# Performance work log

Hardware: AMD Instinct MI355X
Metric: run time of the kernel (lower is better)

## Reference

```python
import jax, jax.numpy as jnp
import numpy as np

BS, IN, HID, LAT, OUT = 8192, 48, 256, 64, 128
CAT = LAT + OUT + HID  # LSTM input size = 448


def setup_inputs() -> dict:
    key = jax.random.key(0)
    ks = jax.random.split(key, 13)
    s = 0.02
    return {
        "x": jax.random.normal(ks[0], (BS, IN), jnp.float32),
        "enc": jax.random.normal(ks[1], (BS, HID), jnp.float32),
        "z": jax.random.normal(ks[2], (BS, LAT), jnp.float32),
        "W_ih": jax.random.normal(ks[3], (4 * OUT, CAT), jnp.float32) * s,
        "W_hh": jax.random.normal(ks[4], (4 * OUT, OUT), jnp.float32) * s,
        "b_ih": jax.random.normal(ks[5], (4 * OUT,), jnp.float32) * s,
        "b_hh": jax.random.normal(ks[6], (4 * OUT,), jnp.float32) * s,
        "W_u0": jax.random.normal(ks[7], (OUT, IN), jnp.float32) * s,
        "b_u0": jax.random.normal(ks[8], (OUT,), jnp.float32) * s,
        "W_h1": jax.random.normal(ks[9], (OUT, CAT), jnp.float32) * s,
        "b_h1": jax.random.normal(ks[10], (OUT,), jnp.float32) * s,
        "W_h2": jax.random.normal(ks[11], (OUT, CAT), jnp.float32) * s,
        "b_h2": jax.random.normal(ks[12], (OUT,), jnp.float32) * s,
        "horizon": 50,
    }


def reference(x, enc, z, W_ih, W_hh, b_ih, b_hh, W_u0, b_u0, W_h1, b_h1, W_h2, b_h2, horizon):
    # initial input u0 = Linear(input_size -> output_size)(x)
    u0 = x @ W_u0.T + b_u0                       # [bs, OUT]
    xi0 = jnp.concatenate([z, u0, enc], axis=-1)  # [bs, CAT]
    h0 = xi0 @ W_h1.T + b_h1                     # LSTM hidden init [bs, OUT]
    c0 = xi0 @ W_h2.T + b_h2                     # LSTM cell init   [bs, OUT]
    b = b_ih + b_hh

    def step(carry, _):
        h, c, yi = carry
        xi = jnp.concatenate([z, yi, enc], axis=-1)   # [bs, CAT]
        gates = xi @ W_ih.T + h @ W_hh.T + b          # [bs, 4*OUT]
        i_g, f_g, g_g, o_g = jnp.split(gates, 4, axis=-1)  # torch order: i,f,g,o
        c_new = jax.nn.sigmoid(f_g) * c + jax.nn.sigmoid(i_g) * jnp.tanh(g_g)
        h_new = jax.nn.sigmoid(o_g) * jnp.tanh(c_new)
        return (h_new, c_new, h_new), h_new

    _, ys = jax.lax.scan(step, (h0, c0, u0), None, length=horizon)  # [T, bs, OUT]
    # torch stacks yi [bs, 1, OUT] along dim=1 -> [bs, T, 1, OUT]
    return jnp.transpose(ys, (1, 0, 2))[:, :, None, :]
```

## Files before the change

### kernel.cpp

```cpp
#include <hip/hip_runtime.h>
#include <stdint.h>

typedef short bf16x8 __attribute__((ext_vector_type(8)));
typedef float f32x4 __attribute__((ext_vector_type(4)));
typedef unsigned short u16x4 __attribute__((ext_vector_type(4)));

#define MFMA16(a,b,c) __builtin_amdgcn_mfma_f32_16x16x32_bf16((a),(b),(c),0,0,0)

__device__ __forceinline__ unsigned short bf16_rne(float f){
  unsigned int u = __builtin_bit_cast(unsigned int, f);
  return (unsigned short)((u + 0x7FFFu + ((u>>16)&1u)) >> 16);
}
__device__ __forceinline__ float bf16_f(unsigned short h){
  unsigned int u = ((unsigned int)h) << 16;
  return __builtin_bit_cast(float, u);
}

#define SZ_WINIT (48*24*512*2)
#define OFF_W0   (SZ_WINIT)
#define SZ_W0    (32*12*512*2)
#define OFF_WC   (OFF_W0 + SZ_W0)
#define SZ_WC    (32*8*512*2)
#define OFF_BIAS (OFF_WC + SZ_WC)
#define OFF_XQ   (OFF_BIAS + 4096)
#define OFF_XH   (OFF_XQ + 512*49*4)

__global__ __launch_bounds__(256)
void decoder_compose(const float* __restrict__ W_ih, const float* __restrict__ W_u0,
                     const float* __restrict__ b_u0, const float* __restrict__ W_h1,
                     const float* __restrict__ W_h2, float* __restrict__ ws){
  __shared__ float wu[128][49];
  __shared__ float wrow[16][128];
  float* Xq = (float*)((char*)ws + OFF_XQ);
  float* Xh = (float*)((char*)ws + OFF_XH);
  const int b = blockIdx.x, tid = threadIdx.x;
  for (int i = tid; i < 128*49; i += 256){
    int c = i/49, j = i - c*49;
    wu[c][j] = (j < 48) ? W_u0[c*48 + j] : b_u0[c];
  }
  for (int i = tid; i < 16*128; i += 256){
    int r = i>>7, c = i&127;
    const float* src;
    if (b < 32) src = W_ih + (b*16 + r)*448 + 64;
    else { int mm = (b-32)*16 + r; src = (mm<128) ? (W_h1 + mm*448 + 64) : (W_h2 + (mm-128)*448 + 64); }
    wrow[r][c] = src[c];
  }
  __syncthreads();
  for (int o = tid; o < 16*49; o += 256){
    int r = o/49, j = o - r*49;
    float s = 0.f;
    #pragma unroll 8
    for (int c = 0; c < 128; ++c) s += wrow[r][c]*wu[c][j];
    if (b < 32) Xq[(b*16+r)*49 + j] = s;
    else        Xh[((b-32)*16+r)*49 + j] = s;
  }
}

__global__ __launch_bounds__(256)
void decoder_pack(const float* __restrict__ W_ih, const float* __restrict__ W_hh,
                  const float* __restrict__ b_ih, const float* __restrict__ b_hh,
                  const float* __restrict__ W_h1, const float* __restrict__ W_h2,
                  const float* __restrict__ b_h1, const float* __restrict__ b_h2,
                  unsigned short* __restrict__ wsu, float* __restrict__ ws){
  const float* Xq = (const float*)((const char*)ws + OFF_XQ);
  const float* Xh = (const float*)((const char*)ws + OFF_XH);
  float* bias = (float*)((char*)ws + OFF_BIAS);
  const int gid = blockIdx.x*256 + threadIdx.x;
  const int slot = gid >> 6, lane = gid & 63;
  const int n16 = lane & 15, p = lane >> 4;

  float v[8];
  unsigned short* dh; unsigned short* dl;
  if (slot < 576) {
    int nt = slot/12, kt = slot - nt*12;
    int n = nt*16 + n16;
    #pragma unroll
    for (int j=0;j<8;++j){
      int k = kt*32 + p*8 + j;
      float xv = 0.f;
      if (n < 256) {
        const float* W = (n<128) ? (W_h1 + n*448) : (W_h2 + (n-128)*448);
        if (k < 64) xv = W[k];
        else if (k < 320) xv = W[192 + k - 64];
        else if (k < 368) xv = Xh[n*49 + (k-320)];
      } else {
        int m = n - 256;
        if (k < 64) xv = W_ih[m*448 + k];
        else if (k < 320) xv = W_ih[m*448 + 192 + k - 64];
      }
      v[j] = xv;
    }
    dh = wsu + ((nt*24 + kt)*64 + lane)*8;
    dl = wsu + ((nt*24 + 12 + kt)*64 + lane)*8;
  } else if (slot < 768) {
    int s2 = slot - 576;
    int nt = s2/6, kt = s2 - nt*6;
    int n = nt*16 + n16;
    #pragma unroll
    for (int j=0;j<8;++j){
      int k = kt*32 + p*8 + j;
      float xv = 0.f;
      if (k < 49)      xv = Xq[n*49 + k];
      else if (k >= 64) xv = W_hh[n*128 + k - 64];
      v[j] = xv;
    }
    unsigned short* b = wsu + OFF_W0/2;
    dh = b + ((nt*12 + kt)*64 + lane)*8;
    dl = b + ((nt*12 + 6 + kt)*64 + lane)*8;
  } else if (slot < 896) {
    int s3 = slot - 768;
    int nt = s3>>2, kt = s3&3;
    int n = nt*16 + n16;
    #pragma unroll
    for (int j=0;j<8;++j){
      int k = kt*32 + p*8 + j;
      v[j] = W_ih[n*448 + 64 + k] + W_hh[n*128 + k];
    }
    unsigned short* b = wsu + OFF_WC/2;
    dh = b + ((nt*8 + kt)*64 + lane)*8;
    dl = b + ((nt*8 + 4 + kt)*64 + lane)*8;
  } else {
    int i = gid - 896*64;
    if (i < 768) {
      float bv;
      if (i < 128)      bv = b_h1[i] + Xh[i*49 + 48];
      else if (i < 256) bv = b_h2[i-128] + Xh[i*49 + 48];
      else              bv = b_ih[i-256] + b_hh[i-256];
      bias[i] = bv;
    }
    return;
  }
  bf16x8 vh, vl;
  #pragma unroll
  for (int j=0;j<8;++j){
    unsigned short h = bf16_rne(v[j]);
    vh[j] = (short)h;
    vl[j] = (short)bf16_rne(v[j] - bf16_f(h));
  }
  *(bf16x8*)dh = vh;
  *(bf16x8*)dl = vl;
}

#define LDS_A0H 0
#define LDS_A0L 12288
#define LDS_XIH 24576
#define LDS_XIL 49152
#define LDS_H   24576
#define LDS_TOTAL 73728

__global__ __launch_bounds__(512, 2)
void decoder_main(const float* __restrict__ x, const float* __restrict__ enc, const float* __restrict__ z,
                  const unsigned short* __restrict__ wsu, const float* __restrict__ bias,
                  const int* __restrict__ hz, float* __restrict__ out){
  extern __shared__ char smem[];
  const int tid = threadIdx.x;
  const int w = tid>>6, lane = tid&63, n16 = lane&15, p = lane>>4;
  const int p16 = p*16;
  const int R0 = blockIdx.x*32;
  const int T = hz[0];

  for (int i = tid; i < 32*384; i += 512){
    int r = i/384, c = i - r*384;
    float v;
    if (c < 64)       v = z[(R0+r)*64 + c];
    else if (c < 320) v = enc[(R0+r)*256 + c - 64];
    else if (c < 368) v = x[(R0+r)*48 + c - 320];
    else              v = 0.f;
    unsigned short h = bf16_rne(v);
    int off = r*768 + ((2*c) ^ ((r&7)<<4));
    *(unsigned short*)(smem + LDS_XIH + off) = h;
    *(unsigned short*)(smem + LDS_XIL + off) = bf16_rne(v - bf16_f(h));
  }
  for (int i = tid; i < 32*64; i += 512){
    int r = i>>6, c = i&63;
    float v = (c < 48) ? x[(R0+r)*48 + c] : (c == 48 ? 1.f : 0.f);
    unsigned short h = bf16_rne(v);
    int off = r*384 + ((2*c) ^ ((r&7)<<4));
    *(unsigned short*)(smem + LDS_A0H + off) = h;
    *(unsigned short*)(smem + LDS_A0L + off) = bf16_rne(v - bf16_f(h));
  }
  __syncthreads();

  const int row0 = n16, row1 = 16 + n16;
  const int s0 = (row0&7)<<4, s1 = (row1&7)<<4;

  f32x4 accs[6][2];
  #pragma unroll
  for (int i=0;i<6;++i){
    int nt = (i==0) ? w : (i==1) ? (8+w) : (16 + 8*(i-2) + w);
    f32x4 bv = *(const f32x4*)(bias + nt*16 + p*4);
    accs[i][0] = bv; accs[i][1] = bv;
  }
  #pragma unroll
  for (int kt=0; kt<12; ++kt){
    bf16x8 bh0 = *(const bf16x8*)(smem + LDS_XIH + row0*768 + ((kt*64 + p16) ^ s0));
    bf16x8 bh1 = *(const bf16x8*)(smem + LDS_XIH + row1*768 + ((kt*64 + p16) ^ s1));
    bf16x8 bl0 = *(const bf16x8*)(smem + LDS_XIL + row0*768 + ((kt*64 + p16) ^ s0));
    bf16x8 bl1 = *(const bf16x8*)(smem + LDS_XIL + row1*768 + ((kt*64 + p16) ^ s1));
    bf16x8 wa[6], wl[6];
    #pragma unroll
    for (int i=0;i<6;++i){
      if (kt >= 10 && i >= 2) continue;
      int nt = (i==0) ? w : (i==1) ? (8+w) : (16 + 8*(i-2) + w);
      wa[i] = *(const bf16x8*)(wsu + ((nt*24 + kt)*64 + lane)*8);
      wl[i] = *(const bf16x8*)(wsu + ((nt*24 + 12 + kt)*64 + lane)*8);
    }
    #pragma unroll
    for (int i=0;i<6;++i){ if (kt >= 10 && i >= 2) continue;
      accs[i][0] = MFMA16(wa[i], bh0, accs[i][0]);
      accs[i][1] = MFMA16(wa[i], bh1, accs[i][1]); }
    #pragma unroll
    for (int i=0;i<6;++i){ if (kt >= 10 && i >= 2) continue;
      accs[i][0] = MFMA16(wa[i], bl0, accs[i][0]);
      accs[i][1] = MFMA16(wa[i], bl1, accs[i][1]); }
    #pragma unroll
    for (int i=0;i<6;++i){ if (kt >= 10 && i >= 2) continue;
      accs[i][0] = MFMA16(wl[i], bh0, accs[i][0]);
      accs[i][1] = MFMA16(wl[i], bh1, accs[i][1]); }
  }
  __syncthreads();

  #pragma unroll
  for (int bt=0; bt<2; ++bt){
    int row = bt*16 + n16, s = (row&7)<<4;
    u16x4 vh, vl;
    #pragma unroll
    for (int e=0;e<4;++e){
      float hv = accs[0][bt][e];
      unsigned short h = bf16_rne(hv);
      vh[e] = h; vl[e] = bf16_rne(hv - bf16_f(h));
    }
    int off = row*384 + ((128 + 32*w + 8*p) ^ s);
    *(u16x4*)(smem + LDS_A0H + off) = vh;
    *(u16x4*)(smem + LDS_A0L + off) = vl;
  }
  f32x4 creg[2] = { accs[1][0], accs[1][1] };
  f32x4 base_r[2][4];
  #pragma unroll
  for (int q=0;q<4;++q){ base_r[0][q] = accs[2+q][0]; base_r[1][q] = accs[2+q][1]; }
  __syncthreads();

  float* outp0 = out + (size_t)(R0 + n16)      * (size_t)(T*128) + (16*w + 4*p);
  float* outp1 = out + (size_t)(R0 + 16 + n16) * (size_t)(T*128) + (16*w + 4*p);

  f32x4 acc[2][4];
  f32x4 hcur0, hcur1;
  const float K1 = 1.44269504088896340736f;
  const float K2 = 2.88539008177792681472f;

  auto lstm_tail = [&](int wb){
    #pragma unroll
    for (int bt=0; bt<2; ++bt){
      f32x4 hh;
      #pragma unroll
      for (int e=0;e<4;++e){
        float iv = acc[bt][0][e], fv = acc[bt][1][e], gv = acc[bt][2][e], ov = acc[bt][3][e];
        float c = creg[bt][e];
        float ef = __builtin_amdgcn_exp2f(-K1*fv);
        float sf = __builtin_amdgcn_rcpf(1.f + ef);
        float ei = __builtin_amdgcn_exp2f(-K1*iv);
        float eg = __builtin_amdgcn_exp2f(-K2*gv);
        float d  = __builtin_amdgcn_rcpf((1.f+ei)*(1.f+eg));
        c = sf*c + (1.f-eg)*d;
        float eo = __builtin_amdgcn_exp2f(-K1*ov);
        float ec = __builtin_amdgcn_exp2f(-K2*c);
        float h  = (1.f-ec)*__builtin_amdgcn_rcpf((1.f+eo)*(1.f+ec));
        creg[bt][e] = c; hh[e] = h;
      }
      if (bt == 0) hcur0 = hh; else hcur1 = hh;
      int row = bt*16 + n16, s = (row&7)<<4;
      u16x4 ph, pl;
      #pragma unroll
      for (int e=0;e<4;++e){
        unsigned short h = bf16_rne(hh[e]);
        ph[e] = h; pl[e] = bf16_rne(hh[e] - bf16_f(h));
      }
      int off = row*256 + ((32*w + 8*p) ^ s);
      *(u16x4*)(smem + LDS_H + (wb*2+0)*8192 + off) = ph;
      *(u16x4*)(smem + LDS_H + (wb*2+1)*8192 + off) = pl;
    }
  };

  {
    const unsigned short* W0p = wsu + OFF_W0/2;
    #pragma unroll
    for (int kt=0; kt<6; ++kt){
      bf16x8 bh0 = *(const bf16x8*)(smem + LDS_A0H + row0*384 + ((kt*64 + p16) ^ s0));
      bf16x8 bh1 = *(const bf16x8*)(smem + LDS_A0H + row1*384 + ((kt*64 + p16) ^ s1));
      bf16x8 bl0 = *(const bf16x8*)(smem + LDS_A0L + row0*384 + ((kt*64 + p16) ^ s0));
      bf16x8 bl1 = *(const bf16x8*)(smem + LDS_A0L + row1*384 + ((kt*64 + p16) ^ s1));
      bf16x8 wa[4], wl[4];
      #pragma unroll
      for (int q=0;q<4;++q){
        wa[q] = *(const bf16x8*)(W0p + (((8*q+w)*12 + kt)*64 + lane)*8);
        wl[q] = *(const bf16x8*)(W0p + (((8*q+w)*12 + 6 + kt)*64 + lane)*8);
      }
      #pragma unroll
      for (int q=0;q<4;++q){
        f32x4 c0i = kt ? acc[0][q] : base_r[0][q];
        f32x4 c1i = kt ? acc[1][q] : base_r[1][q];
        acc[0][q] = MFMA16(wa[q], bh0, c0i);
        acc[1][q] = MFMA16(wa[q], bh1, c1i);
      }
      #pragma unroll
      for (int q=0;q<4;++q){
        acc[0][q] = MFMA16(wa[q], bl0, acc[0][q]);
        acc[1][q] = MFMA16(wa[q], bl1, acc[1][q]);
      }
      #pragma unroll
      for (int q=0;q<4;++q){
        acc[0][q] = MFMA16(wl[q], bh0, acc[0][q]);
        acc[1][q] = MFMA16(wl[q], bh1, acc[1][q]);
      }
    }
    lstm_tail(0);
  }

  const unsigned short* WCp = wsu + OFF_WC/2;
  bf16x8 wchi[4][4], wclo[4][4];
  #pragma unroll
  for (int q=0;q<4;++q){
    #pragma unroll
    for (int kt=0;kt<4;++kt){
      wchi[q][kt] = *(const bf16x8*)(WCp + (((8*q+w)*8 + kt)*64 + lane)*8);
      wclo[q][kt] = *(const bf16x8*)(WCp + (((8*q+w)*8 + 4 + kt)*64 + lane)*8);
    }
  }
  __syncthreads();

  for (int t=1; t<T; ++t){
    *(f32x4*)(outp0 + (t-1)*128) = hcur0;
    *(f32x4*)(outp1 + (t-1)*128) = hcur1;
    const int rb = (t-1)&1, wb = t&1;
    const char* hb = smem + LDS_H + rb*2*8192;
    #pragma unroll
    for (int kt=0; kt<4; ++kt){
      bf16x8 bh0 = *(const bf16x8*)(hb + row0*256 + ((kt*64 + p16) ^ s0));
      bf16x8 bh1 = *(const bf16x8*)(hb + row1*256 + ((kt*64 + p16) ^ s1));
      bf16x8 bl0 = *(const bf16x8*)(hb + 8192 + row0*256 + ((kt*64 + p16) ^ s0));
      bf16x8 bl1 = *(const bf16x8*)(hb + 8192 + row1*256 + ((kt*64 + p16) ^ s1));
      #pragma unroll
      for (int q=0;q<4;++q){
        f32x4 c0i = kt ? acc[0][q] : base_r[0][q];
        f32x4 c1i = kt ? acc[1][q] : base_r[1][q];
        acc[0][q] = MFMA16(wchi[q][kt], bh0, c0i);
        acc[1][q] = MFMA16(wchi[q][kt], bh1, c1i);
      }
      #pragma unroll
      for (int q=0;q<4;++q){
        acc[0][q] = MFMA16(wchi[q][kt], bl0, acc[0][q]);
        acc[1][q] = MFMA16(wchi[q][kt], bl1, acc[1][q]);
      }
      #pragma unroll
      for (int q=0;q<4;++q){
        acc[0][q] = MFMA16(wclo[q][kt], bh0, acc[0][q]);
        acc[1][q] = MFMA16(wclo[q][kt], bh1, acc[1][q]);
      }
    }
    lstm_tail(wb);
    __syncthreads();
  }
  *(f32x4*)(outp0 + (T-1)*128) = hcur0;
  *(f32x4*)(outp1 + (T-1)*128) = hcur1;
}

extern "C" void kernel_launch(void* const* d_in, const int* in_sizes, int n_in,
                              void* d_out, int out_size, void* d_ws, size_t ws_size,
                              hipStream_t stream) {
    (void)in_sizes; (void)n_in; (void)out_size; (void)ws_size;
    const float* x    = (const float*)d_in[0];
    const float* enc  = (const float*)d_in[1];
    const float* z    = (const float*)d_in[2];
    const float* W_ih = (const float*)d_in[3];
    const float* W_hh = (const float*)d_in[4];
    const float* b_ih = (const float*)d_in[5];
    const float* b_hh = (const float*)d_in[6];
    const float* W_u0 = (const float*)d_in[7];
    const float* b_u0 = (const float*)d_in[8];
    const float* W_h1 = (const float*)d_in[9];
    const float* b_h1 = (const float*)d_in[10];
    const float* W_h2 = (const float*)d_in[11];
    const float* b_h2 = (const float*)d_in[12];
    const int*   hz   = (const int*)d_in[13];
    float* out = (float*)d_out;
    unsigned short* wsu = (unsigned short*)d_ws;
    float* bias = (float*)((char*)d_ws + OFF_BIAS);
    float* wsf  = (float*)d_ws;

    (void)hipFuncSetAttribute((const void*)decoder_main,
                              hipFuncAttributeMaxDynamicSharedMemorySize, LDS_TOTAL);

    decoder_compose<<<dim3(48), dim3(256), 0, stream>>>(W_ih, W_u0, b_u0, W_h1, W_h2, wsf);
    decoder_pack<<<dim3(227), dim3(256), 0, stream>>>(W_ih, W_hh, b_ih, b_hh,
                                                      W_h1, W_h2, b_h1, b_h2, wsu, wsf);
    decoder_main<<<dim3(256), dim3(512), LDS_TOTAL, stream>>>(x, enc, z, wsu, bias, hz, out);
}
```

Before: 374.9 us.

## Software-pipeline LSTM recurrence across two row groups, use padded LDS

Splits the 32-row block into two 16-row groups and interleaves them, so one group's MFMA gate GEMM overlaps the other group's transcendental LSTM tail. This is meant to hide the serial dependency between matmul and activation within each step. Replaces XOR-swizzled LDS layouts with padded row pitches. Switches the hi/lo bf16 split from round-to-nearest to truncation with packed 32-bit stores. Trade-offs: LDS grows to 80KB, two barriers per iteration instead of one, and truncation slightly changes the numerics.

```diff
diff --git a/kernel.cpp b/kernel.cpp
--- a/kernel.cpp
+++ b/kernel.cpp
@@ -3,7 +3,7 @@
 
 typedef short bf16x8 __attribute__((ext_vector_type(8)));
 typedef float f32x4 __attribute__((ext_vector_type(4)));
-typedef unsigned short u16x4 __attribute__((ext_vector_type(4)));
+typedef unsigned int u32x2 __attribute__((ext_vector_type(2)));
 
 #define MFMA16(a,b,c) __builtin_amdgcn_mfma_f32_16x16x32_bf16((a),(b),(c),0,0,0)
 
@@ -14,6 +14,25 @@
 __device__ __forceinline__ float bf16_f(unsigned short h){
   unsigned int u = ((unsigned int)h) << 16;
   return __builtin_bit_cast(float, u);
+}
+
+__device__ __forceinline__ void trunc_split_pack(const f32x4& hv, u32x2& ph, u32x2& pl){
+  unsigned b0=__builtin_bit_cast(unsigned,hv[0]);
+  unsigned b1=__builtin_bit_cast(unsigned,hv[1]);
+  unsigned b2=__builtin_bit_cast(unsigned,hv[2]);
+  unsigned b3=__builtin_bit_cast(unsigned,hv[3]);
+  ph[0]=(b1&0xFFFF0000u)|(b0>>16);
+  ph[1]=(b3&0xFFFF0000u)|(b2>>16);
+  float r0=hv[0]-__builtin_bit_cast(float,b0&0xFFFF0000u);
+  float r1=hv[1]-__builtin_bit_cast(float,b1&0xFFFF0000u);
+  float r2=hv[2]-__builtin_bit_cast(float,b2&0xFFFF0000u);
+  float r3=hv[3]-__builtin_bit_cast(float,b3&0xFFFF0000u);
+  unsigned c0=__builtin_bit_cast(unsigned,r0);
+  unsigned c1=__builtin_bit_cast(unsigned,r1);
+  unsigned c2=__builtin_bit_cast(unsigned,r2);
+  unsigned c3=__builtin_bit_cast(unsigned,r3);
+  pl[0]=(c1&0xFFFF0000u)|(c0>>16);
+  pl[1]=(c3&0xFFFF0000u)|(c2>>16);
 }
 
 #define SZ_WINIT (48*24*512*2)
@@ -141,17 +160,21 @@
   *(bf16x8*)dl = vl;
 }
 
+#define P_H   272
+#define P_A0  400
+#define P_XI  784
 #define LDS_A0H 0
-#define LDS_A0L 12288
-#define LDS_XIH 24576
-#define LDS_XIL 49152
-#define LDS_H   24576
-#define LDS_TOTAL 73728
-
-__global__ __launch_bounds__(512, 2)
-void decoder_main(const float* __restrict__ x, const float* __restrict__ enc, const float* __restrict__ z,
-                  const unsigned short* __restrict__ wsu, const float* __restrict__ bias,
-                  const int* __restrict__ hz, float* __restrict__ out){
+#define LDS_A0L 12800
+#define LDS_XIH 25600
+#define LDS_XIL 50688
+#define LDS_HB  25600
+#define LDS_ALLOC 81920
+
+__global__ __launch_bounds__(512) __attribute__((amdgpu_waves_per_eu(2, 2)))
+void decoder_main(const float* __restrict__ x, const float* __restrict__ enc,
+                  const float* __restrict__ z, const unsigned short* __restrict__ wsu,
+                  const float* __restrict__ bias, const int* __restrict__ hz,
+                  float* __restrict__ out){
   extern __shared__ char smem[];
   const int tid = threadIdx.x;
   const int w = tid>>6, lane = tid&63, n16 = lane&15, p = lane>>4;
@@ -167,22 +190,17 @@
     else if (c < 368) v = x[(R0+r)*48 + c - 320];
     else              v = 0.f;
     unsigned short h = bf16_rne(v);
-    int off = r*768 + ((2*c) ^ ((r&7)<<4));
-    *(unsigned short*)(smem + LDS_XIH + off) = h;
-    *(unsigned short*)(smem + LDS_XIL + off) = bf16_rne(v - bf16_f(h));
+    *(unsigned short*)(smem + LDS_XIH + r*P_XI + 2*c) = h;
+    *(unsigned short*)(smem + LDS_XIL + r*P_XI + 2*c) = bf16_rne(v - bf16_f(h));
   }
   for (int i = tid; i < 32*64; i += 512){
     int r = i>>6, c = i&63;
     float v = (c < 48) ? x[(R0+r)*48 + c] : (c == 48 ? 1.f : 0.f);
     unsigned short h = bf16_rne(v);
-    int off = r*384 + ((2*c) ^ ((r&7)<<4));
-    *(unsigned short*)(smem + LDS_A0H + off) = h;
-    *(unsigned short*)(smem + LDS_A0L + off) = bf16_rne(v - bf16_f(h));
+    *(unsigned short*)(smem + LDS_A0H + r*P_A0 + 2*c) = h;
+    *(unsigned short*)(smem + LDS_A0L + r*P_A0 + 2*c) = bf16_rne(v - bf16_f(h));
   }
   __syncthreads();
-
-  const int row0 = n16, row1 = 16 + n16;
-  const int s0 = (row0&7)<<4, s1 = (row1&7)<<4;
 
   f32x4 accs[6][2];
   #pragma unroll
@@ -193,10 +211,10 @@
   }
   #pragma unroll
   for (int kt=0; kt<12; ++kt){
-    bf16x8 bh0 = *(const bf16x8*)(smem + LDS_XIH + row0*768 + ((kt*64 + p16) ^ s0));
-    bf16x8 bh1 = *(const bf16x8*)(smem + LDS_XIH + row1*768 + ((kt*64 + p16) ^ s1));
-    bf16x8 bl0 = *(const bf16x8*)(smem + LDS_XIL + row0*768 + ((kt*64 + p16) ^ s0));
-    bf16x8 bl1 = *(const bf16x8*)(smem + LDS_XIL + row1*768 + ((kt*64 + p16) ^ s1));
+    bf16x8 bh0 = *(const bf16x8*)(smem + LDS_XIH + n16*P_XI      + kt*64 + p16);
+    bf16x8 bh1 = *(const bf16x8*)(smem + LDS_XIH + (16+n16)*P_XI + kt*64 + p16);
+    bf16x8 bl0 = *(const bf16x8*)(smem + LDS_XIL + n16*P_XI      + kt*64 + p16);
+    bf16x8 bl1 = *(const bf16x8*)(smem + LDS_XIL + (16+n16)*P_XI + kt*64 + p16);
     bf16x8 wa[6], wl[6];
     #pragma unroll
     for (int i=0;i<6;++i){
@@ -218,66 +236,56 @@
       accs[i][0] = MFMA16(wl[i], bh0, accs[i][0]);
       accs[i][1] = MFMA16(wl[i], bh1, accs[i][1]); }
   }
+
+  #pragma unroll
+  for (int g=0; g<2; ++g){
+    u32x2 ph, pl;
+    trunc_split_pack(accs[0][g], ph, pl);
+    int off = (g*16 + n16)*P_A0 + 128 + 32*w + 8*p;
+    *(u32x2*)(smem + LDS_A0H + off) = ph;
+    *(u32x2*)(smem + LDS_A0L + off) = pl;
+  }
+  f32x4 creg0 = accs[1][0], creg1 = accs[1][1];
+  f32x4 base0[4], base1[4];
+  #pragma unroll
+  for (int q=0;q<4;++q){ base0[q] = accs[2+q][0]; base1[q] = accs[2+q][1]; }
   __syncthreads();
 
-  #pragma unroll
-  for (int bt=0; bt<2; ++bt){
-    int row = bt*16 + n16, s = (row&7)<<4;
-    u16x4 vh, vl;
-    #pragma unroll
-    for (int e=0;e<4;++e){
-      float hv = accs[0][bt][e];
-      unsigned short h = bf16_rne(hv);
-      vh[e] = h; vl[e] = bf16_rne(hv - bf16_f(h));
-    }
-    int off = row*384 + ((128 + 32*w + 8*p) ^ s);
-    *(u16x4*)(smem + LDS_A0H + off) = vh;
-    *(u16x4*)(smem + LDS_A0L + off) = vl;
-  }
-  f32x4 creg[2] = { accs[1][0], accs[1][1] };
-  f32x4 base_r[2][4];
-  #pragma unroll
-  for (int q=0;q<4;++q){ base_r[0][q] = accs[2+q][0]; base_r[1][q] = accs[2+q][1]; }
-  __syncthreads();
-
-  float* outp0 = out + (size_t)(R0 + n16)      * (size_t)(T*128) + (16*w + 4*p);
-  float* outp1 = out + (size_t)(R0 + 16 + n16) * (size_t)(T*128) + (16*w + 4*p);
-
-  f32x4 acc[2][4];
+  char* h0H = smem + LDS_HB;
+  char* h0L = smem + LDS_HB + 4352;
+  char* h1H = smem + LDS_HB + 8704;
+  char* h1L = smem + LDS_HB + 13056;
+
+  f32x4 acc0[4], acc1[4];
   f32x4 hcur0, hcur1;
   const float K1 = 1.44269504088896340736f;
   const float K2 = 2.88539008177792681472f;
 
-  auto lstm_tail = [&](int wb){
-    #pragma unroll
-    for (int bt=0; bt<2; ++bt){
-      f32x4 hh;
-      #pragma unroll
-      for (int e=0;e<4;++e){
-        float iv = acc[bt][0][e], fv = acc[bt][1][e], gv = acc[bt][2][e], ov = acc[bt][3][e];
-        float c = creg[bt][e];
-        float ef = __builtin_amdgcn_exp2f(-K1*fv);
-        float sf = __builtin_amdgcn_rcpf(1.f + ef);
-        float ei = __builtin_amdgcn_exp2f(-K1*iv);
-        float eg = __builtin_amdgcn_exp2f(-K2*gv);
-        float d  = __builtin_amdgcn_rcpf((1.f+ei)*(1.f+eg));
-        c = sf*c + (1.f-eg)*d;
-        float eo = __builtin_amdgcn_exp2f(-K1*ov);
-        float ec = __builtin_amdgcn_exp2f(-K2*c);
-        float h  = (1.f-ec)*__builtin_amdgcn_rcpf((1.f+eo)*(1.f+ec));
-        creg[bt][e] = c; hh[e] = h;
-      }
-      if (bt == 0) hcur0 = hh; else hcur1 = hh;
-      int row = bt*16 + n16, s = (row&7)<<4;
-      u16x4 ph, pl;
-      #pragma unroll
-      for (int e=0;e<4;++e){
-        unsigned short h = bf16_rne(hh[e]);
-        ph[e] = h; pl[e] = bf16_rne(hh[e] - bf16_f(h));
-      }
-      int off = row*256 + ((32*w + 8*p) ^ s);
-      *(u16x4*)(smem + LDS_H + (wb*2+0)*8192 + off) = ph;
-      *(u16x4*)(smem + LDS_H + (wb*2+1)*8192 + off) = pl;
+  auto tailg = [&](const f32x4 (&ag)[4], f32x4 &cr, f32x4 &hc,
+                   char* hbH, char* hbL, bool wr){
+    f32x4 hv;
+    #pragma unroll
+    for (int e=0;e<4;++e){
+      float iv = ag[0][e], fv = ag[1][e], gv = ag[2][e], ov = ag[3][e];
+      float c = cr[e];
+      float ef = __builtin_amdgcn_exp2f(-K1*fv);
+      float sf = __builtin_amdgcn_rcpf(1.f + ef);
+      float ei = __builtin_amdgcn_exp2f(-K1*iv);
+      float eg = __builtin_amdgcn_exp2f(-K2*gv);
+      float d  = __builtin_amdgcn_rcpf((1.f+ei)*(1.f+eg));
+      c = sf*c + (1.f-eg)*d;
+      float eo = __builtin_amdgcn_exp2f(-K1*ov);
+      float ec = __builtin_amdgcn_exp2f(-K2*c);
+      float h  = (1.f-ec)*__builtin_amdgcn_rcpf((1.f+eo)*(1.f+ec));
+      cr[e] = c; hv[e] = h;
+    }
+    hc = hv;
+    u32x2 ph, pl;
+    trunc_split_pack(hv, ph, pl);
+    if (wr){
+      int off = n16*P_H + 32*w + 8*p;
+      *(u32x2*)(hbH + off) = ph;
+      *(u32x2*)(hbL + off) = pl;
     }
   };
 
@@ -285,36 +293,34 @@
     const unsigned short* W0p = wsu + OFF_W0/2;
     #pragma unroll
     for (int kt=0; kt<6; ++kt){
-      bf16x8 bh0 = *(const bf16x8*)(smem + LDS_A0H + row0*384 + ((kt*64 + p16) ^ s0));
-      bf16x8 bh1 = *(const bf16x8*)(smem + LDS_A0H + row1*384 + ((kt*64 + p16) ^ s1));
-      bf16x8 bl0 = *(const bf16x8*)(smem + LDS_A0L + row0*384 + ((kt*64 + p16) ^ s0));
-      bf16x8 bl1 = *(const bf16x8*)(smem + LDS_A0L + row1*384 + ((kt*64 + p16) ^ s1));
-      bf16x8 wa[4], wl[4];
+      bf16x8 bh0 = *(const bf16x8*)(smem + LDS_A0H + n16*P_A0      + kt*64 + p16);
+      bf16x8 bh1 = *(const bf16x8*)(smem + LDS_A0H + (16+n16)*P_A0 + kt*64 + p16);
+      bf16x8 bl0 = *(const bf16x8*)(smem + LDS_A0L + n16*P_A0      + kt*64 + p16);
+      bf16x8 bl1 = *(const bf16x8*)(smem + LDS_A0L + (16+n16)*P_A0 + kt*64 + p16);
+      bf16x8 wh[4], wl[4];
       #pragma unroll
       for (int q=0;q<4;++q){
-        wa[q] = *(const bf16x8*)(W0p + (((8*q+w)*12 + kt)*64 + lane)*8);
+        wh[q] = *(const bf16x8*)(W0p + (((8*q+w)*12 + kt)*64 + lane)*8);
         wl[q] = *(const bf16x8*)(W0p + (((8*q+w)*12 + 6 + kt)*64 + lane)*8);
       }
       #pragma unroll
       for (int q=0;q<4;++q){
-        f32x4 c0i = kt ? acc[0][q] : base_r[0][q];
-        f32x4 c1i = kt ? acc[1][q] : base_r[1][q];
-        acc[0][q] = MFMA16(wa[q], bh0, c0i);
-        acc[1][q] = MFMA16(wa[q], bh1, c1i);
+        acc0[q] = MFMA16(wh[q], bh0, kt ? acc0[q] : base0[q]);
+        acc1[q] = MFMA16(wh[q], bh1, kt ? acc1[q] : base1[q]);
       }
       #pragma unroll
       for (int q=0;q<4;++q){
-        acc[0][q] = MFMA16(wa[q], bl0, acc[0][q]);
-        acc[1][q] = MFMA16(wa[q], bl1, acc[1][q]);
+        acc0[q] = MFMA16(wh[q], bl0, acc0[q]);
+        acc1[q] = MFMA16(wh[q], bl1, acc1[q]);
       }
       #pragma unroll
       for (int q=0;q<4;++q){
-        acc[0][q] = MFMA16(wl[q], bh0, acc[0][q]);
-        acc[1][q] = MFMA16(wl[q], bh1, acc[1][q]);
-      }
-    }
-    lstm_tail(0);
-  }
+        acc0[q] = MFMA16(wl[q], bh0, acc0[q]);
+        acc1[q] = MFMA16(wl[q], bh1, acc1[q]);
+      }
+    }
+  }
+  tailg(acc0, creg0, hcur0, h0H, h0L, true);
 
   const unsigned short* WCp = wsu + OFF_WC/2;
   bf16x8 wchi[4][4], wclo[4][4];
@@ -328,40 +334,42 @@
   }
   __syncthreads();
 
+  auto gphase = [&](f32x4 (&ag)[4], const f32x4 (&bs)[4], const char* hH, const char* hL){
+    #pragma unroll
+    for (int kt=0; kt<4; ++kt){
+      bf16x8 bh = *(const bf16x8*)(hH + n16*P_H + kt*64 + p16);
+      bf16x8 bl = *(const bf16x8*)(hL + n16*P_H + kt*64 + p16);
+      if (kt == 0){
+        #pragma unroll
+        for (int q=0;q<4;++q) ag[q] = MFMA16(wchi[q][0], bh, bs[q]);
+      } else {
+        #pragma unroll
+        for (int q=0;q<4;++q) ag[q] = MFMA16(wchi[q][kt], bh, ag[q]);
+      }
+      #pragma unroll
+      for (int q=0;q<4;++q) ag[q] = MFMA16(wchi[q][kt], bl, ag[q]);
+      #pragma unroll
+      for (int q=0;q<4;++q) ag[q] = MFMA16(wclo[q][kt], bh, ag[q]);
+    }
+  };
+
+  float* op0 = out + (size_t)(R0 + n16)      * (size_t)(T*128) + (16*w + 4*p);
+  float* op1 = out + (size_t)(R0 + 16 + n16) * (size_t)(T*128) + (16*w + 4*p);
+
   for (int t=1; t<T; ++t){
-    *(f32x4*)(outp0 + (t-1)*128) = hcur0;
-    *(f32x4*)(outp1 + (t-1)*128) = hcur1;
-    const int rb = (t-1)&1, wb = t&1;
-    const char* hb = smem + LDS_H + rb*2*8192;
-    #pragma unroll
-    for (int kt=0; kt<4; ++kt){
-      bf16x8 bh0 = *(const bf16x8*)(hb + row0*256 + ((kt*64 + p16) ^ s0));
-      bf16x8 bh1 = *(const bf16x8*)(hb + row1*256 + ((kt*64 + p16) ^ s1));
-      bf16x8 bl0 = *(const bf16x8*)(hb + 8192 + row0*256 + ((kt*64 + p16) ^ s0));
-      bf16x8 bl1 = *(const bf16x8*)(hb + 8192 + row1*256 + ((kt*64 + p16) ^ s1));
-      #pragma unroll
-      for (int q=0;q<4;++q){
-        f32x4 c0i = kt ? acc[0][q] : base_r[0][q];
-        f32x4 c1i = kt ? acc[1][q] : base_r[1][q];
-        acc[0][q] = MFMA16(wchi[q][kt], bh0, c0i);
-        acc[1][q] = MFMA16(wchi[q][kt], bh1, c1i);
-      }
-      #pragma unroll
-      for (int q=0;q<4;++q){
-        acc[0][q] = MFMA16(wchi[q][kt], bl0, acc[0][q]);
-        acc[1][q] = MFMA16(wchi[q][kt], bl1, acc[1][q]);
-      }
-      #pragma unroll
-      for (int q=0;q<4;++q){
-        acc[0][q] = MFMA16(wclo[q][kt], bh0, acc[0][q]);
-        acc[1][q] = MFMA16(wclo[q][kt], bh1, acc[1][q]);
-      }
-    }
-    lstm_tail(wb);
+    *(f32x4*)op0 = hcur0; op0 += 128;
+    gphase(acc0, base0, h0H, h0L);
+    tailg(acc1, creg1, hcur1, h1H, h1L, true);
     __syncthreads();
-  }
-  *(f32x4*)(outp0 + (T-1)*128) = hcur0;
-  *(f32x4*)(outp1 + (T-1)*128) = hcur1;
+
+    *(f32x4*)op1 = hcur1; op1 += 128;
+    gphase(acc1, base1, h1H, h1L);
+    tailg(acc0, creg0, hcur0, h0H, h0L, true);
+    __syncthreads();
+  }
+  *(f32x4*)op0 = hcur0;
+  tailg(acc1, creg1, hcur1, h1H, h1L, false);
+  *(f32x4*)op1 = hcur1;
 }
 
 extern "C" void kernel_launch(void* const* d_in, const int* in_sizes, int n_in,
@@ -388,10 +396,10 @@
     float* wsf  = (float*)d_ws;
 
     (void)hipFuncSetAttribute((const void*)decoder_main,
-                              hipFuncAttributeMaxDynamicSharedMemorySize, LDS_TOTAL);
+                              hipFuncAttributeMaxDynamicSharedMemorySize, LDS_ALLOC);
 
     decoder_compose<<<dim3(48), dim3(256), 0, stream>>>(W_ih, W_u0, b_u0, W_h1, W_h2, wsf);
     decoder_pack<<<dim3(227), dim3(256), 0, stream>>>(W_ih, W_hh, b_ih, b_hh,
                                                       W_h1, W_h2, b_h1, b_h2, wsu, wsf);
-    decoder_main<<<dim3(256), dim3(512), LDS_TOTAL, stream>>>(x, enc, z, wsu, bias, hz, out);
-}
+    decoder_main<<<dim3(256), dim3(512), LDS_ALLOC, stream>>>(x, enc, z, wsu, bias, hz, out);
+}
```

Result: faster. 364.2 us (-2.8%).
